# Kernel optimization log

Measured on AMD Instinct MI355X. Metric: run time of the kernel, lower is better.

The kernel has to match this reference:

```python
import jax, jax.numpy as jnp
import numpy as np

EPS_CB = 1e-6   # ConvBlock norm_layer eps
EPS_LVC = 1e-5  # default BatchNorm2d/1d eps in LVC branch


def _conv(x, w, stride=1, pad=0):
    return jax.lax.conv_general_dilated(
        x, w, (stride, stride), [(pad, pad), (pad, pad)],
        dimension_numbers=("NCHW", "OIHW", "NCHW"))


def _bn2d(x, g, b, eps):
    # inference-style BN with running_mean=0, running_var=1
    inv = 1.0 / jnp.sqrt(1.0 + eps)
    return x * (g * inv)[None, :, None, None] + b[None, :, None, None]


def setup_inputs() -> dict:
    key = jax.random.key(0)
    ks = jax.random.split(key, 24)
    B, C, Cm, K, H, W = 32, 512, 128, 64, 32, 32
    rn = lambda k, s, sc=0.05: jax.random.normal(k, s, dtype=jnp.float32) * sc
    std = 1.0 / (K * C) ** 0.5
    return {
        "x": jax.random.normal(ks[0], (B, C, H, W), dtype=jnp.float32),
        "c1_w": rn(ks[1], (Cm, C, 1, 1)),
        "bn1_g": 1.0 + rn(ks[2], (Cm,)), "bn1_b": rn(ks[3], (Cm,)),
        "c2_w": rn(ks[4], (Cm, Cm, 3, 3)),
        "bn2_g": 1.0 + rn(ks[5], (Cm,)), "bn2_b": rn(ks[6], (Cm,)),
        "c3_w": rn(ks[7], (C, Cm, 1, 1)),
        "bn3_g": 1.0 + rn(ks[8], (C,)), "bn3_b": rn(ks[9], (C,)),
        "rc_w": rn(ks[10], (C, C, 1, 1)),
        "rbn_g": 1.0 + rn(ks[11], (C,)), "rbn_b": rn(ks[12], (C,)),
        "lvc_w": rn(ks[13], (C, C, 1, 1)),
        "lvcbn_g": 1.0 + rn(ks[14], (C,)), "lvcbn_b": rn(ks[15], (C,)),
        "codewords": jax.random.uniform(ks[16], (K, C), minval=-std, maxval=std, dtype=jnp.float32),
        "scale": jax.random.uniform(ks[17], (K,), minval=-1.0, maxval=0.0, dtype=jnp.float32),
        "enbn_g": 1.0 + rn(ks[18], (K,)), "enbn_b": rn(ks[19], (K,)),
        "fc_w": rn(ks[20], (C, C)), "fc_b": rn(ks[21], (C,)),
    }


def reference(x, c1_w, bn1_g, bn1_b, c2_w, bn2_g, bn2_b, c3_w, bn3_g, bn3_b,
              rc_w, rbn_g, rbn_b, lvc_w, lvcbn_g, lvcbn_b,
              codewords, scale, enbn_g, enbn_b, fc_w, fc_b):
    # ---- ConvBlock (ResNet bottleneck with residual 1x1 conv) ----
    h = jax.nn.relu(_bn2d(_conv(x, c1_w), bn1_g, bn1_b, EPS_CB))
    h = jax.nn.relu(_bn2d(_conv(h, c2_w, pad=1), bn2_g, bn2_b, EPS_CB))
    h = _bn2d(_conv(h, c3_w), bn3_g, bn3_b, EPS_CB)
    r = _bn2d(_conv(x, rc_w), rbn_g, rbn_b, EPS_CB)
    xb = jax.nn.relu(h + r)  # (B,C,H,W)

    # ---- LVC: 1x1 conv + BN + ReLU, then Encoding ----
    e = jax.nn.relu(_bn2d(_conv(xb, lvc_w), lvcbn_g, lvcbn_b, EPS_LVC))
    B, C, H, W = e.shape
    ef = e.reshape(B, C, H * W).transpose(0, 2, 1)  # (B,N,C)

    x2 = jnp.sum(ef * ef, axis=-1)                       # (B,N)
    c2 = jnp.sum(codewords * codewords, axis=-1)         # (K,)
    xc = jnp.einsum("bnc,kc->bnk", ef, codewords)        # (B,N,K)
    sl2 = scale[None, None, :] * (x2[:, :, None] - 2.0 * xc + c2[None, None, :])
    a = jax.nn.softmax(sl2, axis=2)                      # (B,N,K)

    # aggregate: sum_n a_{nk} (x_n - c_k)
    enc = jnp.einsum("bnk,bnc->bkc", a, ef) \
          - jnp.sum(a, axis=1)[:, :, None] * codewords[None, :, :]  # (B,K,C)

    # BatchNorm1d over the K (channel) axis, inference-style, then ReLU
    inv = 1.0 / jnp.sqrt(1.0 + EPS_LVC)
    enc = jax.nn.relu(enc * (enbn_g * inv)[None, :, None] + enbn_b[None, :, None])
    en = jnp.mean(enc, axis=1)                           # (B,C)

    # ---- SE-style gating ----
    gam = jax.nn.sigmoid(en @ fc_w.T + fc_b)             # (B,C)
    return jax.nn.relu(xb + xb * gam[:, :, None, None])
```

## Files before the change

kernel.cpp:

```cpp
#include <hip/hip_runtime.h>
#include <math.h>

constexpr int BATCH = 32;
constexpr int C     = 512;
constexpr int CM    = 128;
constexpr int KW    = 64;
constexpr int NPIX  = 1024;

typedef unsigned short u16;
typedef __attribute__((ext_vector_type(8))) short bf16x8;
typedef __attribute__((ext_vector_type(4))) float f32x4;
typedef __attribute__((ext_vector_type(4))) unsigned short u16x4;
typedef __attribute__((ext_vector_type(8))) unsigned short u16x8;

__device__ __forceinline__ float bf2f(u16 u) {
    unsigned int v = ((unsigned int)u) << 16;
    return __uint_as_float(v);
}
__device__ __forceinline__ u16 f2bf(float f) {
    unsigned int u = __float_as_uint(f);
    u = u + 0x7FFFu + ((u >> 16) & 1u);
    return (u16)(u >> 16);
}
__device__ __forceinline__ float4 ld4(const float* p) {
    return *reinterpret_cast<const float4*>(p);
}
__device__ __forceinline__ void gload16(const u16* g, u16* l) {
    __builtin_amdgcn_global_load_lds((const __attribute__((address_space(1))) void*)g,
                                     (__attribute__((address_space(3))) void*)l, 16, 0, 0);
}

template<int MODE, int TM, bool RELU, bool WTR>
__global__ __launch_bounds__(256)
void gemm_mfma(const u16* __restrict__ A1, const u16* __restrict__ A2,
               const u16* __restrict__ Wm, u16* __restrict__ outB,
               u16* __restrict__ outT,
               const float* __restrict__ scale, const float* __restrict__ bias,
               const u16* __restrict__ zbuf, int K, int Cout)
{
    constexpr int MF = TM / 32;
    __shared__ __align__(16) u16 As[TM * 64];
    __shared__ __align__(16) u16 Bs[128 * 64];
    const int b   = blockIdx.z;
    const int n0  = blockIdx.x * TM;
    const int co0 = blockIdx.y * 128;
    const int t    = threadIdx.x;
    const int lane = t & 63;
    const int w    = t >> 6;
    const int wr = w >> 1, wc = w & 1;
    const int lhi = lane >> 4, llo = lane & 15;

    f32x4 acc[MF][4];
#pragma unroll
    for (int i = 0; i < MF; ++i)
#pragma unroll
        for (int j = 0; j < 4; ++j) acc[i][j] = (f32x4){0.f, 0.f, 0.f, 0.f};

    for (int k0 = 0; k0 < K; k0 += 64) {
#pragma unroll
        for (int rd = 0; rd < (TM * 8) / 256; ++rd) {
            int ch = t + rd * 256;
            int g  = ch / TM, r = ch % TM;
            int kg = k0 + g * 8;
            const u16* src;
            if (MODE == 0) {
                src = A1 + ((size_t)((b << 10) + n0 + r)) * (size_t)K + kg;
            } else if (MODE == 1) {
                int tap = kg >> 7, ci = kg & 127;
                int n = n0 + r;
                int y = (n >> 5) + tap / 3 - 1;
                int x = (n & 31) + tap % 3 - 1;
                src = ((unsigned)y < 32u && (unsigned)x < 32u)
                    ? A1 + ((size_t)((b << 10) + y * 32 + x)) * 128 + ci
                    : zbuf;
            } else {
                src = (kg < 128)
                    ? A1 + ((size_t)((b << 10) + n0 + r)) * 128 + kg
                    : A2 + ((size_t)((b << 10) + n0 + r)) * 512 + (kg - 128);
            }
            gload16(src, &As[ch * 8]);
        }
#pragma unroll
        for (int rd = 0; rd < 4; ++rd) {
            int ch = t + rd * 256;
            int g = ch >> 7, r = ch & 127;
            gload16(Wm + (size_t)(co0 + r) * (size_t)K + k0 + g * 8, &Bs[ch * 8]);
        }
        __syncthreads();
        const bf16x8* Av = (const bf16x8*)As;
        const bf16x8* Bv = (const bf16x8*)Bs;
#pragma unroll
        for (int kk = 0; kk < 2; ++kk) {
            bf16x8 af[MF], bfr[4];
#pragma unroll
            for (int m = 0; m < MF; ++m)
                af[m] = Av[(kk * 4 + lhi) * TM + wr * (TM / 2) + m * 16 + llo];
#pragma unroll
            for (int nf = 0; nf < 4; ++nf)
                bfr[nf] = Bv[(kk * 4 + lhi) * 128 + wc * 64 + nf * 16 + llo];
#pragma unroll
            for (int m = 0; m < MF; ++m)
#pragma unroll
                for (int nf = 0; nf < 4; ++nf)
                    acc[m][nf] = __builtin_amdgcn_mfma_f32_16x16x32_bf16(af[m], bfr[nf], acc[m][nf], 0, 0, 0);
        }
        __syncthreads();
    }
#pragma unroll
    for (int nf = 0; nf < 4; ++nf) {
        int coL = co0 + wc * 64 + nf * 16 + llo;
        float s  = scale ? scale[coL] : 1.f;
        float bi = bias  ? bias[coL]  : 0.f;
#pragma unroll
        for (int m = 0; m < MF; ++m) {
            f32x4 v = acc[m][nf];
            int rowb = n0 + wr * (TM / 2) + m * 16 + lhi * 4;
            u16 o[4];
#pragma unroll
            for (int q = 0; q < 4; ++q) {
                float val = fmaf(v[q], s, bi);
                if (RELU) val = fmaxf(val, 0.f);
                o[q] = f2bf(val);
                outB[((size_t)((b << 10) + rowb + q)) * (size_t)Cout + coL] = o[q];
            }
            if (WTR) {
                u16x4 ov;
                ov[0] = o[0]; ov[1] = o[1]; ov[2] = o[2]; ov[3] = o[3];
                *(u16x4*)(outT + (((size_t)(b * Cout + coL)) << 10) + rowb) = ov;
            }
        }
    }
}

__global__ __launch_bounds__(256)
void gemm_xc(const u16* __restrict__ e, const u16* __restrict__ cwb,
             const float* __restrict__ scale, const float* __restrict__ c2,
             u16* __restrict__ a_t, float* __restrict__ asum)
{
    const int b  = blockIdx.y;
    const int n0 = blockIdx.x * 64;
    const int t    = threadIdx.x;
    const int lane = t & 63;
    const int w    = t >> 6;
    const int wr = w >> 1, wc = w & 1;
    const int lhi = lane >> 4, llo = lane & 15;

    __shared__ __align__(16) char smem[16640];
    u16* As = (u16*)smem;
    u16* Bs = (u16*)(smem + 4096);
    float (*sm)[65] = (float(*)[65])smem;
    __shared__ float x2s[64], pmax[64][4], psum[64][4], sc_s[64], c2_s[64];
    if (t < 64) { sc_s[t] = scale[t]; c2_s[t] = c2[t]; }

    f32x4 acc[2][2];
#pragma unroll
    for (int i = 0; i < 2; ++i)
#pragma unroll
        for (int j = 0; j < 2; ++j) acc[i][j] = (f32x4){0.f, 0.f, 0.f, 0.f};
    float x2p = 0.f;
    const int aBase = lhi * 64 + wr * 32 + llo;
    const int bBase = lhi * 64 + wc * 32 + llo;
    const int xr = w * 16 + (lane >> 2);
    const int xg = lane & 3;

    const int g = t >> 6, r = t & 63;
    for (int k0 = 0; k0 < 512; k0 += 32) {
        gload16(e + ((size_t)((b << 10) + n0 + r)) * 512 + k0 + g * 8, &As[t * 8]);
        gload16(cwb + (size_t)r * 512 + k0 + g * 8, &Bs[t * 8]);
        __syncthreads();
        {
            u16x8 vv = *(const u16x8*)&As[(xg * 64 + xr) * 8];
#pragma unroll
            for (int j = 0; j < 8; ++j) { float f = bf2f(vv[j]); x2p = fmaf(f, f, x2p); }
        }
        const bf16x8* Av = (const bf16x8*)As;
        const bf16x8* Bv = (const bf16x8*)Bs;
        bf16x8 af[2], bfr[2];
#pragma unroll
        for (int m = 0; m < 2; ++m)  af[m]  = Av[aBase + m * 16];
#pragma unroll
        for (int nf = 0; nf < 2; ++nf) bfr[nf] = Bv[bBase + nf * 16];
#pragma unroll
        for (int m = 0; m < 2; ++m)
#pragma unroll
            for (int nf = 0; nf < 2; ++nf)
                acc[m][nf] = __builtin_amdgcn_mfma_f32_16x16x32_bf16(af[m], bfr[nf], acc[m][nf], 0, 0, 0);
        __syncthreads();
    }
    float xs = x2p + __shfl_xor(x2p, 1, 64);
    xs += __shfl_xor(xs, 2, 64);
    if ((lane & 3) == 0) x2s[xr] = xs;
    __syncthreads();
#pragma unroll
    for (int m = 0; m < 2; ++m)
#pragma unroll
        for (int nf = 0; nf < 2; ++nf)
#pragma unroll
            for (int q = 0; q < 4; ++q) {
                int rr = wr * 32 + m * 16 + lhi * 4 + q;
                int cc = wc * 32 + nf * 16 + llo;
                sm[rr][cc] = sc_s[cc] * (x2s[rr] - 2.f * acc[m][nf][q] + c2_s[cc]);
            }
    __syncthreads();
    const int gq = t >> 6;
    float vloc[16];
    float pm = -1e30f;
#pragma unroll
    for (int j = 0; j < 16; ++j) { float v = sm[r][gq * 16 + j]; vloc[j] = v; pm = fmaxf(pm, v); }
    pmax[r][gq] = pm;
    __syncthreads();
    float mm = fmaxf(fmaxf(pmax[r][0], pmax[r][1]), fmaxf(pmax[r][2], pmax[r][3]));
    float ps = 0.f;
#pragma unroll
    for (int j = 0; j < 16; ++j) { float p = __expf(vloc[j] - mm); vloc[j] = p; ps += p; }
    psum[r][gq] = ps;
    __syncthreads();
    float inv = 1.f / (psum[r][0] + psum[r][1] + psum[r][2] + psum[r][3]);
#pragma unroll
    for (int j = 0; j < 16; ++j) {
        int k = gq * 16 + j;
        float av = vloc[j] * inv;
        a_t[((size_t)((b << 6) + k) << 10) + n0 + r] = f2bf(av);
        sm[r][k] = av;
    }
    __syncthreads();
    const int kk = t & 63, rg = t >> 6;
    float pa = 0.f;
#pragma unroll
    for (int j = 0; j < 16; ++j) pa += sm[rg * 16 + j][kk];
    atomicAdd(&asum[(b << 6) + kk], pa);
}

__global__ __launch_bounds__(256)
void enc_mfma(const u16* __restrict__ a_t, const u16* __restrict__ e_t,
              const float* __restrict__ cw, const float* __restrict__ asum,
              const float* __restrict__ sK, const float* __restrict__ bK,
              float* __restrict__ en)
{
    const int b  = blockIdx.y;
    const int c0 = blockIdx.x * 64;
    const int t    = threadIdx.x;
    const int lane = t & 63;
    const int w    = t >> 6;
    const int lhi = lane >> 4, llo = lane & 15;
    __shared__ __align__(16) u16 As[2048];
    __shared__ __align__(16) u16 Bs[2048];
    f32x4 acc[4];
#pragma unroll
    for (int i = 0; i < 4; ++i) acc[i] = (f32x4){0.f, 0.f, 0.f, 0.f};
    const int aBase = lhi * 64 + llo;
    const int bBase = lhi * 64 + w * 16 + llo;
    const int g = t >> 6, r = t & 63;

    for (int n0 = 0; n0 < NPIX; n0 += 32) {
        gload16(a_t + ((size_t)((b << 6) + r) << 10) + n0 + g * 8, &As[t * 8]);
        gload16(e_t + ((size_t)((b << 9) + c0 + r) << 10) + n0 + g * 8, &Bs[t * 8]);
        __syncthreads();
        const bf16x8* Av = (const bf16x8*)As;
        const bf16x8* Bv = (const bf16x8*)Bs;
        bf16x8 bfr = Bv[bBase];
#pragma unroll
        for (int m = 0; m < 4; ++m)
            acc[m] = __builtin_amdgcn_mfma_f32_16x16x32_bf16(Av[aBase + m * 16], bfr, acc[m], 0, 0, 0);
        __syncthreads();
    }
    const int c = c0 + w * 16 + llo;
    float s = 0.f;
#pragma unroll
    for (int m = 0; m < 4; ++m)
#pragma unroll
        for (int q = 0; q < 4; ++q) {
            int k = m * 16 + lhi * 4 + q;
            float v = acc[m][q] - asum[(b << 6) + k] * cw[((size_t)k << 9) + c];
            v = fmaxf(fmaf(v, sK[k], bK[k]), 0.f);
            s += v;
        }
    s += __shfl_xor(s, 16, 64);
    s += __shfl_xor(s, 32, 64);
    if (lane < 16) en[(size_t)(b << 9) + c] = s * (1.f / 64.f);
}

__global__ __launch_bounds__(256)
void tr_in_k(const float* __restrict__ x, u16* __restrict__ xbf)
{
    __shared__ float tile[64][65];
    int b = blockIdx.z, n0 = blockIdx.x * 64, c0 = blockIdx.y * 64, t = threadIdx.x;
#pragma unroll
    for (int q = 0; q < 16; ++q) {
        int idx = t + 256 * q;
        int c = idx >> 6, n = idx & 63;
        tile[c][n] = x[((size_t)((b << 9) + c0 + c) << 10) + n0 + n];
    }
    __syncthreads();
#pragma unroll
    for (int q = 0; q < 16; ++q) {
        int idx = t + 256 * q;
        int nn = idx >> 6, cc = idx & 63;
        xbf[((size_t)((b << 10) + n0 + nn) << 9) + c0 + cc] = f2bf(tile[cc][nn]);
    }
}

__global__ __launch_bounds__(256)
void final_tr_k(const u16* __restrict__ xb, const float* __restrict__ gam,
                float* __restrict__ out)
{
    __shared__ float tile[64][65];
    int b = blockIdx.z, n0 = blockIdx.x * 64, c0 = blockIdx.y * 64, t = threadIdx.x;
#pragma unroll
    for (int q = 0; q < 16; ++q) {
        int idx = t + 256 * q;
        int n = idx >> 6, c = idx & 63;
        float gm = 1.f + gam[(b << 9) + c0 + c];
        float v = bf2f(xb[((size_t)((b << 10) + n0 + n) << 9) + c0 + c]) * gm;
        tile[n][c] = fmaxf(v, 0.f);
    }
    __syncthreads();
#pragma unroll
    for (int q = 0; q < 16; ++q) {
        int idx = t + 256 * q;
        int cc = idx >> 6, nn = idx & 63;
        out[((size_t)((b << 9) + c0 + cc) << 10) + n0 + nn] = tile[nn][cc];
    }
}

__global__ __launch_bounds__(256)
void gam_k(const float* __restrict__ en, const float* __restrict__ fcw,
           const float* __restrict__ fcb, float* __restrict__ gam)
{
    int b = blockIdx.x;
    int c = blockIdx.y * 256 + threadIdx.x;
    __shared__ float es[C];
    es[threadIdx.x]       = en[(size_t)b * C + threadIdx.x];
    es[threadIdx.x + 256] = en[(size_t)b * C + threadIdx.x + 256];
    __syncthreads();
    float s = fcb[c];
    const float* wp = fcw + (size_t)c * C;
    for (int i = 0; i < C; i += 4) {
        float4 wv = ld4(wp + i);
        s = fmaf(es[i], wv.x, s);
        s = fmaf(es[i + 1], wv.y, s);
        s = fmaf(es[i + 2], wv.z, s);
        s = fmaf(es[i + 3], wv.w, s);
    }
    gam[(size_t)b * C + c] = 1.f / (1.f + __expf(-s));
}

__global__ __launch_bounds__(256)
void prep_all_k(const float* c1w, const float* bn1g, const float* bn2g,
                const float* c2w, const float* c3w, const float* bn3g,
                const float* bn3b, const float* rcw, const float* rbng,
                const float* rbnb, const float* lvcw, const float* lvcbng,
                const float* enbng, const float* cw,
                u16* c1b, u16* w2b, u16* wcatb, u16* lvcb, u16* cwb,
                float* s1, float* s2, float* slvc, float* bcat,
                float* sK, float* c2, float* asum, u16* zbuf)
{
    const float invCB  = rsqrtf(1.f + 1e-6f);
    const float invLVC = rsqrtf(1.f + 1e-5f);
    long id = (long)blockIdx.x * 256 + threadIdx.x;
    if (id < 327680) {
        int co = (int)(id / 640), k = (int)(id % 640);
        float v = (k < 128) ? c3w[co * 128 + k] * (bn3g[co] * invCB)
                            : rcw[co * 512 + (k - 128)] * (rbng[co] * invCB);
        wcatb[id] = f2bf(v);
        return;
    }
    id -= 327680;
    if (id < 147456) {
        int co = (int)(id / 1152), k = (int)(id % 1152);
        int tap = k >> 7, ci = k & 127;
        w2b[id] = f2bf(c2w[co * 1152 + ci * 9 + tap]);
        return;
    }
    id -= 147456;
    if (id < 262144) { lvcb[id] = f2bf(lvcw[id]); return; }
    id -= 262144;
    if (id < 65536)  { c1b[id]  = f2bf(c1w[id]);  return; }
    id -= 65536;
    if (id < 32768)  { cwb[id]  = f2bf(cw[id]);   return; }
    id -= 32768;
    if (id < 2048)   { asum[id] = 0.f; return; }
    id -= 2048;
    if (id < 1024)   { zbuf[id] = 0;   return; }
    id -= 1024;
    if (id < 128) { s1[id] = bn1g[id] * invCB; return; }
    id -= 128;
    if (id < 128) { s2[id] = bn2g[id] * invCB; return; }
    id -= 128;
    if (id < 512) { slvc[id] = lvcbng[id] * invLVC; return; }
    id -= 512;
    if (id < 512) { bcat[id] = bn3b[id] + rbnb[id]; return; }
    id -= 512;
    if (id < 64)  { sK[id] = enbng[id] * invLVC; return; }
    id -= 64;
    if (id < 64) {
        float s = 0.f;
        for (int c = 0; c < C; ++c) s = fmaf(cw[id * C + c], cw[id * C + c], s);
        c2[id] = s;
    }
}

extern "C" void kernel_launch(void* const* d_in, const int* in_sizes, int n_in,
                              void* d_out, int out_size, void* d_ws, size_t ws_size,
                              hipStream_t stream)
{
    const float* x      = (const float*)d_in[0];
    const float* c1w    = (const float*)d_in[1];
    const float* bn1g   = (const float*)d_in[2];
    const float* bn1b   = (const float*)d_in[3];
    const float* c2w    = (const float*)d_in[4];
    const float* bn2g   = (const float*)d_in[5];
    const float* bn2b   = (const float*)d_in[6];
    const float* c3w    = (const float*)d_in[7];
    const float* bn3g   = (const float*)d_in[8];
    const float* bn3b   = (const float*)d_in[9];
    const float* rcw    = (const float*)d_in[10];
    const float* rbng   = (const float*)d_in[11];
    const float* rbnb   = (const float*)d_in[12];
    const float* lvcw   = (const float*)d_in[13];
    const float* lvcbng = (const float*)d_in[14];
    const float* lvcbnb = (const float*)d_in[15];
    const float* cw     = (const float*)d_in[16];
    const float* scale  = (const float*)d_in[17];
    const float* enbng  = (const float*)d_in[18];
    const float* enbnb  = (const float*)d_in[19];
    const float* fcw    = (const float*)d_in[20];
    const float* fcb    = (const float*)d_in[21];
    float* out = (float*)d_out;
    char* W = (char*)d_ws;

    u16*  xbf  = (u16*)(W);
    u16*  e_b  = xbf;
    u16*  h1   = (u16*)(W + 33554432);
    u16*  a_t  = h1;
    u16*  h2   = (u16*)(W + 41943040);
    u16*  xb_b = (u16*)(W + 50331648);
    u16*  e_t  = (u16*)(W + 83886080);
    char* wb   = W + 117440512;
    u16* c1b   = (u16*)(wb);
    u16* w2b   = (u16*)(wb + 131072);
    u16* wcatb = (u16*)(wb + 425984);
    u16* lvcb  = (u16*)(wb + 1081344);
    u16* cwb   = (u16*)(wb + 1605632);
    float* fb  = (float*)(wb + 1671168);
    float* asum = fb;
    float* en   = fb + 2048;
    float* gam  = fb + 18432;
    float* s1   = fb + 34816;
    float* s2   = s1 + 128;
    float* slvc = s2 + 128;
    float* bcat = slvc + 512;
    float* sK   = bcat + 512;
    float* c2   = sK + 64;
    u16* zbuf   = (u16*)(c2 + 64);

    prep_all_k<<<3282, 256, 0, stream>>>(c1w, bn1g, bn2g, c2w, c3w, bn3g, bn3b,
                                         rcw, rbng, rbnb, lvcw, lvcbng, enbng, cw,
                                         c1b, w2b, wcatb, lvcb, cwb,
                                         s1, s2, slvc, bcat, sK, c2, asum, zbuf);

    tr_in_k<<<dim3(16, 8, 32), 256, 0, stream>>>(x, xbf);

    gemm_mfma<0, 64, true, false><<<dim3(16, 1, 32), 256, 0, stream>>>(
        xbf, nullptr, c1b, h1, nullptr, s1, bn1b, zbuf, 512, 128);
    gemm_mfma<1, 64, true, false><<<dim3(16, 1, 32), 256, 0, stream>>>(
        h1, nullptr, w2b, h2, nullptr, s2, bn2b, zbuf, 1152, 128);
    gemm_mfma<2, 128, true, false><<<dim3(8, 4, 32), 256, 0, stream>>>(
        h2, xbf, wcatb, xb_b, nullptr, nullptr, bcat, zbuf, 640, 512);
    gemm_mfma<0, 128, true, true><<<dim3(8, 4, 32), 256, 0, stream>>>(
        xb_b, nullptr, lvcb, e_b, e_t, slvc, lvcbnb, zbuf, 512, 512);
    gemm_xc<<<dim3(16, 32), 256, 0, stream>>>(e_b, cwb, scale, c2, a_t, asum);
    enc_mfma<<<dim3(8, 32), 256, 0, stream>>>(a_t, e_t, cw, asum, sK, enbnb, en);
    gam_k<<<dim3(32, 2), 256, 0, stream>>>(en, fcw, fcb, gam);
    final_tr_k<<<dim3(16, 8, 32), 256, 0, stream>>>(xb_b, gam, out);
}
```

Measured before the change: 384.4 us.

## Double-buffer LDS tiles in MFMA GEMM to overlap global loads with compute

Splits the GEMM K-loop into separate stage and compute steps, using two LDS buffers for A and B, so the next tile's global-to-LDS loads are issued while the current tile is multiplied. Explicit vmcnt waits and barriers replace the per-iteration syncthreads pair. This aims to hide global memory latency behind MFMA work, at the cost of doubled shared memory, which can lower occupancy. It also assumes K/64 is even.

```diff
diff --git a/kernel.cpp b/kernel.cpp
--- a/kernel.cpp
+++ b/kernel.cpp
@@ -38,9 +38,11 @@
                const float* __restrict__ scale, const float* __restrict__ bias,
                const u16* __restrict__ zbuf, int K, int Cout)
 {
-    constexpr int MF = TM / 32;
-    __shared__ __align__(16) u16 As[TM * 64];
-    __shared__ __align__(16) u16 Bs[128 * 64];
+    constexpr int MF  = TM / 32;
+    constexpr int ALD = (TM * 8) / 256;
+    constexpr int LPS = ALD + 4;
+    __shared__ __align__(16) u16 As[2][TM * 64];
+    __shared__ __align__(16) u16 Bs[2][128 * 64];
     const int b   = blockIdx.z;
     const int n0  = blockIdx.x * TM;
     const int co0 = blockIdx.y * 128;
@@ -56,9 +58,9 @@
 #pragma unroll
         for (int j = 0; j < 4; ++j) acc[i][j] = (f32x4){0.f, 0.f, 0.f, 0.f};
 
-    for (int k0 = 0; k0 < K; k0 += 64) {
-#pragma unroll
-        for (int rd = 0; rd < (TM * 8) / 256; ++rd) {
+    auto stage = [&](u16* Ad, u16* Bd, int k0) {
+#pragma unroll
+        for (int rd = 0; rd < ALD; ++rd) {
             int ch = t + rd * 256;
             int g  = ch / TM, r = ch % TM;
             int kg = k0 + g * 8;
@@ -78,17 +80,19 @@
                     ? A1 + ((size_t)((b << 10) + n0 + r)) * 128 + kg
                     : A2 + ((size_t)((b << 10) + n0 + r)) * 512 + (kg - 128);
             }
-            gload16(src, &As[ch * 8]);
+            gload16(src, Ad + ch * 8);
         }
 #pragma unroll
         for (int rd = 0; rd < 4; ++rd) {
             int ch = t + rd * 256;
             int g = ch >> 7, r = ch & 127;
-            gload16(Wm + (size_t)(co0 + r) * (size_t)K + k0 + g * 8, &Bs[ch * 8]);
-        }
-        __syncthreads();
-        const bf16x8* Av = (const bf16x8*)As;
-        const bf16x8* Bv = (const bf16x8*)Bs;
+            gload16(Wm + (size_t)(co0 + r) * (size_t)K + k0 + g * 8, Bd + ch * 8);
+        }
+    };
+
+    auto compute = [&](const u16* Ad, const u16* Bd) {
+        const bf16x8* Av = (const bf16x8*)Ad;
+        const bf16x8* Bv = (const bf16x8*)Bd;
 #pragma unroll
         for (int kk = 0; kk < 2; ++kk) {
             bf16x8 af[MF], bfr[4];
@@ -104,8 +108,33 @@
                 for (int nf = 0; nf < 4; ++nf)
                     acc[m][nf] = __builtin_amdgcn_mfma_f32_16x16x32_bf16(af[m], bfr[nf], acc[m][nf], 0, 0, 0);
         }
-        __syncthreads();
-    }
+    };
+
+    const int nt = K >> 6;
+    stage(As[0], Bs[0], 0);
+    stage(As[1], Bs[1], 64);
+
+    for (int ti = 0; ti < nt; ti += 2) {
+        asm volatile("s_waitcnt vmcnt(%0)" :: "n"(LPS) : "memory");
+        __builtin_amdgcn_s_barrier();
+        __builtin_amdgcn_sched_barrier(0);
+        compute(As[0], Bs[0]);
+        __builtin_amdgcn_sched_barrier(0);
+        __builtin_amdgcn_s_barrier();
+        if (ti + 2 < nt) {
+            stage(As[0], Bs[0], (ti + 2) << 6);
+            asm volatile("s_waitcnt vmcnt(%0)" :: "n"(LPS) : "memory");
+        } else {
+            asm volatile("s_waitcnt vmcnt(0)" ::: "memory");
+        }
+        __builtin_amdgcn_s_barrier();
+        __builtin_amdgcn_sched_barrier(0);
+        compute(As[1], Bs[1]);
+        __builtin_amdgcn_sched_barrier(0);
+        __builtin_amdgcn_s_barrier();
+        if (ti + 3 < nt) stage(As[1], Bs[1], (ti + 3) << 6);
+    }
+
 #pragma unroll
     for (int nf = 0; nf < 4; ++nf) {
         int coL = co0 + wc * 64 + nf * 16 + llo;
```

Result: no change. 377.5 us (-1.8%).
